# Kernel optimization log

Measured on AMD Instinct MI355X. Metric: run time of the kernel, lower is better.

The kernel has to match this reference:

```python
import jax, jax.numpy as jnp
import numpy as np

ORDER = 2
C_IN = 32
C_OUT = 32
SUPPORT_LEN = 2


def setup_inputs() -> dict:
    key = jax.random.key(0)
    k1, k2, k3, k4 = jax.random.split(key, 4)
    B, C, V, L = 32, C_IN, 2048, 12
    x = jax.random.normal(k1, (B, C, V, L), dtype=jnp.float32)
    supports = jax.random.uniform(k2, (SUPPORT_LEN, V, V), dtype=jnp.float32) / V
    c_cat = (ORDER * SUPPORT_LEN + 1) * C_IN
    W = jax.random.normal(k3, (C_OUT, c_cat), dtype=jnp.float32) * (1.0 / np.sqrt(c_cat))
    b = jax.random.normal(k4, (C_OUT,), dtype=jnp.float32) * 0.01
    return {"x": x, "supports": supports, "W": W, "b": b}


def reference(x, supports, W, b):
    # x: [B, C, V, L]; supports: [S, V, V]; W: [c_out, (order*S+1)*C]; b: [c_out]
    out = [x]
    for s in range(supports.shape[0]):  # fixed small S
        A = supports[s]
        x1 = jnp.einsum('bcvl,vw->bcwl', x, A)
        out.append(x1)
        for _ in range(ORDER - 1):
            x1 = jnp.einsum('bcvl,vw->bcwl', x1, A)
            out.append(x1)
    h = jnp.concatenate(out, axis=1)  # [B, (order*S+1)*C, V, L]
    # 1x1 conv == channel-mixing matmul; dropout is identity in eval mode
    y = jnp.einsum('bcvl,oc->bovl', h, W) + b[None, :, None, None]
    return y
```

## Files before the change

### kernel.cpp

```cpp
#include <hip/hip_runtime.h>

#define BB 32
#define CC 32
#define VV 2048
#define LL 12
#define NCOL 12288
#define MMEGA 8192
#define VB ((size_t)VV * VV)

typedef __attribute__((ext_vector_type(8))) short bf16x8;
typedef __attribute__((ext_vector_type(4))) float f32x4;

__device__ __forceinline__ unsigned short f2b(float f) {
    union { float f; unsigned u; } v; v.f = f;
    unsigned u = v.u;
    unsigned r = (u + 0x7fffu + ((u >> 16) & 1u)) >> 16;
    return (unsigned short)r;
}
__device__ __forceinline__ float b2f(unsigned short h) {
    union { unsigned u; float f; } v; v.u = ((unsigned)h) << 16;
    return v.f;
}

__device__ __forceinline__ void stg(const unsigned short* g, unsigned short* l) {
    __builtin_amdgcn_global_load_lds((const __attribute__((address_space(1))) void*)g,
                                     (__attribute__((address_space(3))) void*)l, 16, 0, 0);
}

__global__ void k_prepA(const float* __restrict__ A,
                        unsigned short* __restrict__ Abf,
                        unsigned short* __restrict__ Gt) {
    __shared__ float t[32][33];
    const int s = blockIdx.z;
    const float* As = A + (size_t)s * VB;
    const int w0 = blockIdx.x * 32, v0 = blockIdx.y * 32;
    const int tid = threadIdx.x;
    const int cc = tid & 31;
    unsigned short* Ao = Abf + (size_t)s * VB;
#pragma unroll
    for (int i = 0; i < 4; i++) {
        int rr = (tid >> 5) + i * 8;
        float val = As[(size_t)(v0 + rr) * VV + w0 + cc];
        t[rr][cc] = val;
        Ao[(size_t)(v0 + rr) * VV + w0 + cc] = f2b(val);
    }
    __syncthreads();
    unsigned short* G = Gt + (size_t)(2 * s) * VB;
#pragma unroll
    for (int i = 0; i < 4; i++) {
        int rr = (tid >> 5) + i * 8;
        G[(size_t)(w0 + rr) * VV + v0 + cc] = f2b(t[cc][rr]);
    }
}

__global__ void k_transpose_x(const float* __restrict__ x,
                              unsigned short* __restrict__ Xb) {
    __shared__ float t[128 * 13];
    const int bc = blockIdx.y;
    const int v0 = blockIdx.x * 128;
    const float* xs = x + (size_t)bc * VV * LL + (size_t)v0 * LL;
    const int tid = threadIdx.x;
#pragma unroll
    for (int i = 0; i < 6; i++) {
        int e = tid + i * 256;
        int col = e / 12, row = e - col * 12;
        t[col * 13 + row] = xs[e];
    }
    __syncthreads();
    unsigned short* X = Xb + (size_t)bc * LL * VV + v0;
#pragma unroll
    for (int i = 0; i < 2; i++) {
        int flat = tid + i * 256;
        if (flat < 384) {
            int row = flat >> 5;
            int col = (flat & 31) * 4;
            ushort4 o;
            o.x = f2b(t[(col + 0) * 13 + row]);
            o.y = f2b(t[(col + 1) * 13 + row]);
            o.z = f2b(t[(col + 2) * 13 + row]);
            o.w = f2b(t[(col + 3) * 13 + row]);
            *(ushort4*)&X[(size_t)row * VV + col] = o;
        }
    }
}

template<bool F32OUT>
__device__ __forceinline__ void gemm_core(const unsigned short* __restrict__ Ag,
                                          const unsigned short* __restrict__ Bg,
                                          void* __restrict__ Cg,
                                          int ld, int Kloc, int koff,
                                          int m0, int n0, int ldc)
{
    __shared__ unsigned short SH[65536];
    const int tid  = threadIdx.x;
    const int lane = tid & 63;
    const int wid  = tid >> 6;
    const int wr   = wid >> 2;
    const int wc   = wid & 3;
    const int fr   = lane & 15;
    const int g    = lane >> 4;
    const int NT   = Kloc >> 6;

    const unsigned short* gA = Ag + (size_t)m0 * ld + koff;
    const unsigned short* gB = Bg + (size_t)n0 * ld + koff;

    const int lrow  = lane >> 3;
    const int lslot = (lane & 7) ^ lrow;
    const size_t laneGOff = (size_t)lrow * ld + lslot * 8;

    const int qa  = wid * 16;
    const int rA0 = (qa & 63) + ((qa & 64) << 1);
    const int rA1 = ((qa + 8) & 63) + (((qa + 8) & 64) << 1);
    const int rB0 = (qa & 31) + ((qa & ~31) << 1);
    const int rB1 = ((qa + 8) & 31) + (((qa + 8) & ~31) << 1);

    const int frlow = fr & 7;
    const int sw0 = ((0 + g) ^ frlow) << 4;
    const int sw1 = ((4 + g) ^ frlow) << 4;
    const int aOffB = (wr * 128 + fr) * 128;
    const int bOffB = (wc * 64  + fr) * 128;

    f32x4 acc[8][4];
#pragma unroll
    for (int i = 0; i < 8; ++i)
#pragma unroll
        for (int j = 0; j < 4; ++j) { f32x4 z = {0.f, 0.f, 0.f, 0.f}; acc[i][j] = z; }

#define STG_A(Lb, rb, kt) stg(gA + (size_t)(rb) * ld + ((size_t)(kt) << 6) + laneGOff, (Lb) + (rb) * 64)
#define STG_B(Lb, rb, kt) stg(gB + (size_t)(rb) * ld + ((size_t)(kt) << 6) + laneGOff, (Lb) + (rb) * 64)
#define ST_Aa(Lb, kt) do { if ((kt) < NT) { STG_A(Lb, rA0, kt);      STG_A(Lb, rA1, kt);      } } while (0)
#define ST_Ab(Lb, kt) do { if ((kt) < NT) { STG_A(Lb, rA0 + 64, kt); STG_A(Lb, rA1 + 64, kt); } } while (0)
#define ST_Ba(Lb, kt) do { if ((kt) < NT) { STG_B(Lb, rB0, kt);      STG_B(Lb, rB1, kt);      } } while (0)
#define ST_Bb(Lb, kt) do { if ((kt) < NT) { STG_B(Lb, rB0 + 32, kt); STG_B(Lb, rB1 + 32, kt); } } while (0)
#define VM6() asm volatile("s_waitcnt vmcnt(6)" ::: "memory")
#define VM0() asm volatile("s_waitcnt vmcnt(0)" ::: "memory")
#define LGKM(n) asm volatile("s_waitcnt lgkmcnt(" #n ")" ::: "memory")
#define SCHB() __builtin_amdgcn_sched_barrier(0)
#define SBAR() __builtin_amdgcn_s_barrier()

    unsigned short* A0L = SH;
    unsigned short* B0L = SH + 16384;
    unsigned short* A1L = SH + 32768;
    unsigned short* B1L = SH + 49152;

    ST_Aa(A0L, 0); ST_Ab(A0L, 0); ST_Ba(B0L, 0); ST_Bb(B0L, 0);
    ST_Aa(A1L, 1); ST_Ab(A1L, 1); ST_Ba(B1L, 1);
    if (NT > 1) { VM6(); } else { VM0(); }
    SBAR();

    bf16x8 aA[4][2], aB[4][2], b0[2][2], b1[2][2];
    {
        const char* Ab = (const char*)SH;
        const char* Bb = Ab + 32768;
#pragma unroll
        for (int i = 0; i < 4; ++i) {
            aA[i][0] = *(const bf16x8*)(Ab + aOffB + i * 2048 + sw0);
            aA[i][1] = *(const bf16x8*)(Ab + aOffB + i * 2048 + sw1);
        }
#pragma unroll
        for (int j = 0; j < 2; ++j) {
            b0[j][0] = *(const bf16x8*)(Bb + bOffB + j * 2048 + sw0);
            b0[j][1] = *(const bf16x8*)(Bb + bOffB + j * 2048 + sw1);
        }
    }

    for (int t = 0; t < NT; ++t) {
        const char* Ab  = (const char*)(SH + ((t & 1) << 15));
        const char* Bb  = Ab + 32768;
        const char* AbN = (const char*)(SH + (((t + 1) & 1) << 15));
        const char* BbN = AbN + 32768;
        unsigned short* An = SH + (((t + 1) & 1) << 15);
        unsigned short* Bn = An + 16384;
        unsigned short* Ac = SH + ((t & 1) << 15);
        unsigned short* Bc = Ac + 16384;
        (void)An;

#pragma unroll
        for (int i = 0; i < 4; ++i) {
            aB[i][0] = *(const bf16x8*)(Ab + aOffB + 8192 + i * 2048 + sw0);
            aB[i][1] = *(const bf16x8*)(Ab + aOffB + 8192 + i * 2048 + sw1);
        }
        ST_Bb(Bn, t + 1);
        SBAR(); LGKM(8); SCHB();
        __builtin_amdgcn_s_setprio(1);
#pragma unroll
        for (int i = 0; i < 4; ++i)
#pragma unroll
            for (int j = 0; j < 2; ++j) {
                acc[i][j] = __builtin_amdgcn_mfma_f32_16x16x32_bf16(aA[i][0], b0[j][0], acc[i][j], 0, 0, 0);
                acc[i][j] = __builtin_amdgcn_mfma_f32_16x16x32_bf16(aA[i][1], b0[j][1], acc[i][j], 0, 0, 0);
            }
        __builtin_amdgcn_s_setprio(0);
        SBAR();

#pragma unroll
        for (int j = 0; j < 2; ++j) {
            b1[j][0] = *(const bf16x8*)(Bb + bOffB + 4096 + j * 2048 + sw0);
            b1[j][1] = *(const bf16x8*)(Bb + bOffB + 4096 + j * 2048 + sw1);
        }
        ST_Aa(Ac, t + 2);
        SBAR(); LGKM(4); SCHB();
        __builtin_amdgcn_s_setprio(1);
#pragma unroll
        for (int i = 0; i < 4; ++i)
#pragma unroll
            for (int j = 0; j < 2; ++j) {
                acc[4 + i][j] = __builtin_amdgcn_mfma_f32_16x16x32_bf16(aB[i][0], b0[j][0], acc[4 + i][j], 0, 0, 0);
                acc[4 + i][j] = __builtin_amdgcn_mfma_f32_16x16x32_bf16(aB[i][1], b0[j][1], acc[4 + i][j], 0, 0, 0);
            }
        __builtin_amdgcn_s_setprio(0);
        SBAR();

        ST_Ab(Ac, t + 2);
        SBAR(); LGKM(0); SCHB();
        __builtin_amdgcn_s_setprio(1);
#pragma unroll
        for (int i = 0; i < 4; ++i)
#pragma unroll
            for (int j = 0; j < 2; ++j) {
                acc[i][2 + j] = __builtin_amdgcn_mfma_f32_16x16x32_bf16(aA[i][0], b1[j][0], acc[i][2 + j], 0, 0, 0);
                acc[i][2 + j] = __builtin_amdgcn_mfma_f32_16x16x32_bf16(aA[i][1], b1[j][1], acc[i][2 + j], 0, 0, 0);
            }
        __builtin_amdgcn_s_setprio(0);
        SBAR();

        ST_Ba(Bc, t + 2);
        if (t + 2 < NT) { VM6(); } else { VM0(); }
        SBAR();
#pragma unroll
        for (int i = 0; i < 4; ++i) {
            aA[i][0] = *(const bf16x8*)(AbN + aOffB + i * 2048 + sw0);
            aA[i][1] = *(const bf16x8*)(AbN + aOffB + i * 2048 + sw1);
        }
#pragma unroll
        for (int j = 0; j < 2; ++j) {
            b0[j][0] = *(const bf16x8*)(BbN + bOffB + j * 2048 + sw0);
            b0[j][1] = *(const bf16x8*)(BbN + bOffB + j * 2048 + sw1);
        }
        LGKM(12); SCHB();
        __builtin_amdgcn_s_setprio(1);
#pragma unroll
        for (int i = 0; i < 4; ++i)
#pragma unroll
            for (int j = 0; j < 2; ++j) {
                acc[4 + i][2 + j] = __builtin_amdgcn_mfma_f32_16x16x32_bf16(aB[i][0], b1[j][0], acc[4 + i][2 + j], 0, 0, 0);
                acc[4 + i][2 + j] = __builtin_amdgcn_mfma_f32_16x16x32_bf16(aB[i][1], b1[j][1], acc[4 + i][2 + j], 0, 0, 0);
            }
        __builtin_amdgcn_s_setprio(0);
        SBAR();
    }

    const int er = g * 4;
#pragma unroll
    for (int i = 0; i < 8; ++i)
#pragma unroll
        for (int j = 0; j < 4; ++j) {
            int row = m0 + wr * 128 + i * 16 + er;
            int col = n0 + wc * 64 + j * 16 + fr;
#pragma unroll
            for (int r = 0; r < 4; ++r) {
                if (F32OUT)
                    ((float*)Cg)[(size_t)(row + r) * ldc + col] = acc[i][j][r];
                else
                    ((unsigned short*)Cg)[(size_t)(row + r) * ldc + col] = f2b(acc[i][j][r]);
            }
        }
#undef STG_A
#undef STG_B
#undef ST_Aa
#undef ST_Ab
#undef ST_Ba
#undef ST_Bb
#undef VM6
#undef VM0
#undef LGKM
#undef SCHB
#undef SBAR
}

__global__ __launch_bounds__(512, 2) void k_gemm_mega(
    const unsigned short* __restrict__ Ag, const unsigned short* __restrict__ Bg,
    unsigned short* __restrict__ Cg)
{
    const int bid = blockIdx.x;
    const int xcd = bid & 7;
    const int t   = bid >> 3;
    const int sx  = t >> 5;
    const int loc = t & 31;
    const int x = sx * 8 + (loc & 7);
    const int y = xcd * 4 + (loc >> 3);
    gemm_core<false>(Ag, Bg, (void*)Cg, VV, VV, 0, y * 256, x * 256, NCOL);
}

__global__ __launch_bounds__(512, 2) void k_gemm_small(
    const unsigned short* __restrict__ Gt, const unsigned short* __restrict__ Abf,
    float* __restrict__ P)
{
    const int bid = blockIdx.x;
    const int s  = bid >> 7;
    const int kz = (bid >> 6) & 1;
    const int y  = (bid >> 3) & 7;
    const int x  = bid & 7;
    const unsigned short* A = Gt + (size_t)(2 * s) * VB;
    const unsigned short* B = Abf + (size_t)s * VB;
    float* C = P + (size_t)(s * 2 + kz) * VB;
    gemm_core<true>(A, B, (void*)C, VV, 1024, kz * 1024, y * 256, x * 256, VV);
}

__global__ void k_combine(const float* __restrict__ P,
                          unsigned short* __restrict__ Gt) {
    const int s = blockIdx.y;
    size_t i = ((size_t)blockIdx.x * 256 + threadIdx.x) * 4;
    float4 a = *(const float4*)(P + (size_t)(2 * s) * VB + i);
    float4 b = *(const float4*)(P + (size_t)(2 * s + 1) * VB + i);
    ushort4 o;
    o.x = f2b(a.x + b.x); o.y = f2b(a.y + b.y);
    o.z = f2b(a.z + b.z); o.w = f2b(a.w + b.w);
    *(ushort4*)(Gt + (size_t)(2 * s + 1) * VB + i) = o;
}

__global__ __launch_bounds__(192) void k_epilogue(const float* __restrict__ x,
                                                  const unsigned short* __restrict__ U,
                                                  const float* __restrict__ W,
                                                  const float* __restrict__ bias,
                                                  float* __restrict__ y) {
    __shared__ float xs[32][192];
    __shared__ unsigned short us[64][392];
    const int b = blockIdx.y;
    const int w0 = blockIdx.x * 16;
    const int tid = threadIdx.x;

    const float* xp = x + ((size_t)(b * 32) * VV + w0) * LL;
#pragma unroll 4
    for (int c = 0; c < 32; c++)
        xs[c][tid] = xp[(size_t)c * (VV * LL) + tid];

    {
        const int r0 = tid / 48;
        const int c0 = tid - r0 * 48;
#pragma unroll
        for (int it = 0; it < 16; ++it) {
            int r = it * 4 + r0;
            int krow = (r >> 4) * VV + w0 + (r & 15);
            const unsigned short* up = U + (size_t)krow * NCOL + b * 384 + c0 * 8;
            *(bf16x8*)&us[r][c0 * 8] = *(const bf16x8*)up;
        }
    }
    __syncthreads();

    const int w = tid / 12, l = tid - w * 12;
    float acc[32];
#pragma unroll
    for (int o = 0; o < 32; o++) acc[o] = bias[o];

    for (int c = 0; c < 32; c++) {
        float h = xs[c][tid];
#pragma unroll
        for (int o = 0; o < 32; o++) acc[o] += W[o * 160 + c] * h;
    }
    for (int c = 0; c < 32; c++) {
#pragma unroll
        for (int k = 0; k < 4; k++) {
            float h = b2f(us[k * 16 + w][c * 12 + l]);
#pragma unroll
            for (int o = 0; o < 32; o++) acc[o] += W[o * 160 + (k + 1) * 32 + c] * h;
        }
    }

    float* yp = y + ((size_t)(b * 32) * VV + w0) * LL;
#pragma unroll
    for (int o = 0; o < 32; o++)
        yp[(size_t)o * (VV * LL) + tid] = acc[o];
}

extern "C" void kernel_launch(void* const* d_in, const int* in_sizes, int n_in,
                              void* d_out, int out_size, void* d_ws, size_t ws_size,
                              hipStream_t stream) {
    const float* x        = (const float*)d_in[0];
    const float* supports = (const float*)d_in[1];
    const float* W        = (const float*)d_in[2];
    const float* bias     = (const float*)d_in[3];
    float* y = (float*)d_out;

    char* ws = (char*)d_ws;
    unsigned short* Xb  = (unsigned short*)(ws);
    unsigned short* Gt  = (unsigned short*)(ws + 50331648);
    unsigned short* Abf = (unsigned short*)(ws + 83886080);
    unsigned short* U   = (unsigned short*)(ws + 100663296);
    float*          P   = (float*)(ws + 100663296);

    k_prepA<<<dim3(64, 64, 2), 256, 0, stream>>>(supports, Abf, Gt);

    k_gemm_small<<<dim3(256), 512, 0, stream>>>(Gt, Abf, P);

    k_combine<<<dim3(4096, 2), 256, 0, stream>>>(P, Gt);

    k_transpose_x<<<dim3(16, 1024), 256, 0, stream>>>(x, Xb);

    k_gemm_mega<<<dim3(1536), 512, 0, stream>>>(Gt, Xb, U);

    k_epilogue<<<dim3(VV / 16, BB), 192, 0, stream>>>(x, U, W, bias, y);
}
```

Measured before the change: 833.7 us.

## Scatter big GEMM output into per-batch layout and simplify epilogue

```diff
diff --git a/kernel.cpp b/kernel.cpp
--- a/kernel.cpp
+++ b/kernel.cpp
@@ -7,6 +7,7 @@
 #define NCOL 12288
 #define MMEGA 8192
 #define VB ((size_t)VV * VV)
+#define PPB 24576
 
 typedef __attribute__((ext_vector_type(8))) short bf16x8;
 typedef __attribute__((ext_vector_type(4))) float f32x4;
@@ -17,8 +18,8 @@
     unsigned r = (u + 0x7fffu + ((u >> 16) & 1u)) >> 16;
     return (unsigned short)r;
 }
-__device__ __forceinline__ float b2f(unsigned short h) {
-    union { unsigned u; float f; } v; v.u = ((unsigned)h) << 16;
+__device__ __forceinline__ float bits2f(unsigned u) {
+    union { unsigned u; float f; } v; v.u = u;
     return v.f;
 }
 
@@ -84,7 +85,7 @@
     }
 }
 
-template<bool F32OUT>
+template<int OMODE>
 __device__ __forceinline__ void gemm_core(const unsigned short* __restrict__ Ag,
                                           const unsigned short* __restrict__ Bg,
                                           void* __restrict__ Cg,
@@ -251,20 +252,42 @@
     }
 
     const int er = g * 4;
-#pragma unroll
-    for (int i = 0; i < 8; ++i)
+    if (OMODE == 2) {
+        int bcj[4], lj[4];
 #pragma unroll
         for (int j = 0; j < 4; ++j) {
-            int row = m0 + wr * 128 + i * 16 + er;
             int col = n0 + wc * 64 + j * 16 + fr;
-#pragma unroll
-            for (int r = 0; r < 4; ++r) {
-                if (F32OUT)
-                    ((float*)Cg)[(size_t)(row + r) * ldc + col] = acc[i][j][r];
-                else
-                    ((unsigned short*)Cg)[(size_t)(row + r) * ldc + col] = f2b(acc[i][j][r]);
-            }
-        }
+            bcj[j] = col / 12;
+            lj[j]  = col - bcj[j] * 12;
+        }
+#pragma unroll
+        for (int i = 0; i < 8; ++i) {
+            int rowm = m0 + wr * 128 + i * 16 + er;
+            int kb = rowm >> 11, w = rowm & 2047;
+#pragma unroll
+            for (int j = 0; j < 4; ++j) {
+                size_t base = ((size_t)bcj[j] * 4 + kb) * PPB + (size_t)w * 12 + lj[j];
+#pragma unroll
+                for (int r = 0; r < 4; ++r)
+                    ((unsigned short*)Cg)[base + (size_t)r * 12] = f2b(acc[i][j][r]);
+            }
+        }
+    } else {
+#pragma unroll
+        for (int i = 0; i < 8; ++i)
+#pragma unroll
+            for (int j = 0; j < 4; ++j) {
+                int row = m0 + wr * 128 + i * 16 + er;
+                int col = n0 + wc * 64 + j * 16 + fr;
+#pragma unroll
+                for (int r = 0; r < 4; ++r) {
+                    if (OMODE == 1)
+                        ((float*)Cg)[(size_t)(row + r) * ldc + col] = acc[i][j][r];
+                    else
+                        ((unsigned short*)Cg)[(size_t)(row + r) * ldc + col] = f2b(acc[i][j][r]);
+                }
+            }
+    }
 #undef STG_A
 #undef STG_B
 #undef ST_Aa
@@ -289,7 +312,7 @@
     const int loc = t & 31;
     const int x = sx * 8 + (loc & 7);
     const int y = xcd * 4 + (loc >> 3);
-    gemm_core<false>(Ag, Bg, (void*)Cg, VV, VV, 0, y * 256, x * 256, NCOL);
+    gemm_core<2>(Ag, Bg, (void*)Cg, VV, VV, 0, y * 256, x * 256, 0);
 }
 
 __global__ __launch_bounds__(512, 2) void k_gemm_small(
@@ -304,7 +327,7 @@
     const unsigned short* A = Gt + (size_t)(2 * s) * VB;
     const unsigned short* B = Abf + (size_t)s * VB;
     float* C = P + (size_t)(s * 2 + kz) * VB;
-    gemm_core<true>(A, B, (void*)C, VV, 1024, kz * 1024, y * 256, x * 256, VV);
+    gemm_core<1>(A, B, (void*)C, VV, 1024, kz * 1024, y * 256, x * 256, VV);
 }
 
 __global__ void k_combine(const float* __restrict__ P,
@@ -319,58 +342,52 @@
     *(ushort4*)(Gt + (size_t)(2 * s + 1) * VB + i) = o;
 }
 
-__global__ __launch_bounds__(192) void k_epilogue(const float* __restrict__ x,
-                                                  const unsigned short* __restrict__ U,
-                                                  const float* __restrict__ W,
-                                                  const float* __restrict__ bias,
-                                                  float* __restrict__ y) {
-    __shared__ float xs[32][192];
-    __shared__ unsigned short us[64][392];
-    const int b = blockIdx.y;
-    const int w0 = blockIdx.x * 16;
-    const int tid = threadIdx.x;
-
-    const float* xp = x + ((size_t)(b * 32) * VV + w0) * LL;
+__global__ __launch_bounds__(256) void k_epilogue2(const float* __restrict__ x,
+                                                   const unsigned short* __restrict__ Up,
+                                                   const float* __restrict__ W,
+                                                   const float* __restrict__ bias,
+                                                   float* __restrict__ y) {
+    const int gid = blockIdx.x * 256 + threadIdx.x;
+    const int p0 = gid * 2;
+    const int b = p0 / PPB;
+    const int pl = p0 - b * PPB;
+    const float* xp = x + ((size_t)b * 32) * PPB + pl;
+    const unsigned short* up = Up + ((size_t)b * 128) * PPB + pl;
+
+    float a0[32], a1[32];
+#pragma unroll
+    for (int o = 0; o < 32; ++o) { float bv = bias[o]; a0[o] = bv; a1[o] = bv; }
+
 #pragma unroll 4
-    for (int c = 0; c < 32; c++)
-        xs[c][tid] = xp[(size_t)c * (VV * LL) + tid];
-
-    {
-        const int r0 = tid / 48;
-        const int c0 = tid - r0 * 48;
-#pragma unroll
-        for (int it = 0; it < 16; ++it) {
-            int r = it * 4 + r0;
-            int krow = (r >> 4) * VV + w0 + (r & 15);
-            const unsigned short* up = U + (size_t)krow * NCOL + b * 384 + c0 * 8;
-            *(bf16x8*)&us[r][c0 * 8] = *(const bf16x8*)up;
-        }
-    }
-    __syncthreads();
-
-    const int w = tid / 12, l = tid - w * 12;
-    float acc[32];
-#pragma unroll
-    for (int o = 0; o < 32; o++) acc[o] = bias[o];
-
-    for (int c = 0; c < 32; c++) {
-        float h = xs[c][tid];
-#pragma unroll
-        for (int o = 0; o < 32; o++) acc[o] += W[o * 160 + c] * h;
-    }
-    for (int c = 0; c < 32; c++) {
-#pragma unroll
-        for (int k = 0; k < 4; k++) {
-            float h = b2f(us[k * 16 + w][c * 12 + l]);
-#pragma unroll
-            for (int o = 0; o < 32; o++) acc[o] += W[o * 160 + (k + 1) * 32 + c] * h;
-        }
-    }
-
-    float* yp = y + ((size_t)(b * 32) * VV + w0) * LL;
-#pragma unroll
-    for (int o = 0; o < 32; o++)
-        yp[(size_t)o * (VV * LL) + tid] = acc[o];
+    for (int c = 0; c < 32; ++c) {
+        float2 xv = *(const float2*)(xp + (size_t)c * PPB);
+#pragma unroll
+        for (int o = 0; o < 32; ++o) {
+            float wv = W[o * 160 + c];
+            a0[o] += wv * xv.x; a1[o] += wv * xv.y;
+        }
+    }
+#pragma unroll
+    for (int k = 0; k < 4; ++k) {
+#pragma unroll 4
+        for (int c = 0; c < 32; ++c) {
+            unsigned uv = *(const unsigned*)(up + (size_t)(c * 4 + k) * PPB);
+            float u0 = bits2f(uv << 16);
+            float u1 = bits2f(uv & 0xffff0000u);
+#pragma unroll
+            for (int o = 0; o < 32; ++o) {
+                float wv = W[o * 160 + (k + 1) * 32 + c];
+                a0[o] += wv * u0; a1[o] += wv * u1;
+            }
+        }
+    }
+
+    float* yp = y + ((size_t)b * 32) * PPB + pl;
+#pragma unroll
+    for (int o = 0; o < 32; ++o) {
+        float2 ov; ov.x = a0[o]; ov.y = a1[o];
+        *(float2*)(yp + (size_t)o * PPB) = ov;
+    }
 }
 
 extern "C" void kernel_launch(void* const* d_in, const int* in_sizes, int n_in,
@@ -386,7 +403,7 @@
     unsigned short* Xb  = (unsigned short*)(ws);
     unsigned short* Gt  = (unsigned short*)(ws + 50331648);
     unsigned short* Abf = (unsigned short*)(ws + 83886080);
-    unsigned short* U   = (unsigned short*)(ws + 100663296);
+    unsigned short* Up  = (unsigned short*)(ws + 100663296);
     float*          P   = (float*)(ws + 100663296);
 
     k_prepA<<<dim3(64, 64, 2), 256, 0, stream>>>(supports, Abf, Gt);
@@ -397,7 +414,7 @@
 
     k_transpose_x<<<dim3(16, 1024), 256, 0, stream>>>(x, Xb);
 
-    k_gemm_mega<<<dim3(1536), 512, 0, stream>>>(Gt, Xb, U);
-
-    k_epilogue<<<dim3(VV / 16, BB), 192, 0, stream>>>(x, U, W, bias, y);
-}
+    k_gemm_mega<<<dim3(1536), 512, 0, stream>>>(Gt, Xb, Up);
+
+    k_epilogue2<<<dim3(786432 / 512), 256, 0, stream>>>(x, Up, W, bias, y);
+}
```

Result: faster. 741.2 us (-11.1%).
